# Kernel tuning notes

Hardware: AMD Instinct MI355X
Metric: run time of the kernel (lower is better)

Reference implementation:

```python
import jax, jax.numpy as jnp
import numpy as np

N_NODES = 20000
N_EDGES = 160000
N_GRAPHS = 500
F_IN = 128
HID = 512
N_CLS = 10
N_LAYERS = 3
BN_EPS = 1e-5
BN_BIAS = 1e-4  # BatchNorm1d weight init to 1, bias to 0.0001


def bn(x):
    # training-mode BatchNorm1d with gamma=1, beta=1e-4 (per module init)
    m = jnp.mean(x, axis=0)
    v = jnp.mean((x - m) ** 2, axis=0)
    return (x - m) * jax.lax.rsqrt(v + BN_EPS) + BN_BIAS


def gcn_norm(row, col, edge_weight, num_nodes):
    # add self loops with weight 1, symmetric deg^-1/2 normalization
    loop = jnp.arange(num_nodes)
    r = jnp.concatenate([row, loop])
    c = jnp.concatenate([col, loop])
    w = jnp.concatenate([edge_weight, jnp.ones((num_nodes,), edge_weight.dtype)])
    deg = jax.ops.segment_sum(w, r, num_segments=num_nodes)
    dis = jnp.where(deg > 0, jax.lax.rsqrt(deg), jnp.zeros_like(deg))
    return r, c, dis[r] * w * dis[c]


def gcn(x, W, b, r, c, norm):
    # x@W then gather source feats, scale by norm, scatter-add to targets
    h = x @ W
    out = jax.ops.segment_sum(norm[:, None] * h[c], r, num_segments=x.shape[0])
    return out + b


def readout(x, W1, b1, W2, b2):
    x = bn(x) @ W1 + b1
    x = jax.nn.relu(x)
    x = bn(x) @ W2 + b2
    return jax.nn.log_softmax(x, axis=-1)


def setup_inputs() -> dict:
    key = jax.random.key(0)
    ks = iter(jax.random.split(key, 40))

    def lin(k, fin, fout):
        return jax.random.normal(k, (fin, fout), jnp.float32) * (1.0 / np.sqrt(fin))

    x = jax.random.normal(next(ks), (N_NODES, F_IN), jnp.float32)
    edge_index = jax.random.randint(next(ks), (2, N_EDGES), 0, N_NODES)
    batch = jnp.sort(jax.random.randint(next(ks), (N_NODES,), 0, N_GRAPHS))
    perm = jax.random.permutation(next(ks), N_GRAPHS)

    inp = {"x": x, "edge_index": edge_index, "batch": batch, "perm": perm}
    inp["conv_feat_W"] = lin(next(ks), F_IN, HID)
    inp["conv_feat_b"] = jnp.zeros((HID,), jnp.float32)
    inp["convs_W"] = jax.random.normal(next(ks), (N_LAYERS, HID, HID), jnp.float32) * (1.0 / np.sqrt(HID))
    inp["convs_b"] = jnp.zeros((N_LAYERS, HID), jnp.float32)
    inp["edge_att_W"] = lin(next(ks), 2 * HID, 2)
    inp["edge_att_b"] = jnp.zeros((2,), jnp.float32)
    inp["node_att_W"] = lin(next(ks), HID, 2)
    inp["node_att_b"] = jnp.zeros((2,), jnp.float32)
    inp["ctx_W"] = lin(next(ks), HID, HID)
    inp["ctx_b"] = jnp.zeros((HID,), jnp.float32)
    inp["obj_W"] = lin(next(ks), HID, HID)
    inp["obj_b"] = jnp.zeros((HID,), jnp.float32)
    for tag in ("c", "o", "co"):
        inp[f"fc1_{tag}_W"] = lin(next(ks), HID, HID)
        inp[f"fc1_{tag}_b"] = jnp.zeros((HID,), jnp.float32)
        inp[f"fc2_{tag}_W"] = lin(next(ks), HID, N_CLS)
        inp[f"fc2_{tag}_b"] = jnp.zeros((N_CLS,), jnp.float32)
    return inp


def reference(x, edge_index, batch, perm,
              conv_feat_W, conv_feat_b, convs_W, convs_b,
              edge_att_W, edge_att_b, node_att_W, node_att_b,
              ctx_W, ctx_b, obj_W, obj_b,
              fc1_c_W, fc1_c_b, fc2_c_W, fc2_c_b,
              fc1_o_W, fc1_o_b, fc2_o_W, fc2_o_b,
              fc1_co_W, fc1_co_b, fc2_co_W, fc2_co_b):
    row, col = edge_index[0], edge_index[1]
    n = x.shape[0]

    x = bn(x)
    x = jax.nn.relu(x @ conv_feat_W + conv_feat_b)  # conv_feat has gfn=True: pure linear

    # unweighted symmetric norm, shared by all stacked convs
    r1, c1, nrm1 = gcn_norm(row, col, jnp.ones((row.shape[0],), x.dtype), n)
    for i in range(N_LAYERS):
        x = bn(x)
        x = jax.nn.relu(gcn(x, convs_W[i], convs_b[i], r1, c1, nrm1))

    edge_rep = jnp.concatenate([x[row], x[col]], axis=-1)        # [E, 2H]
    edge_att = jax.nn.softmax(edge_rep @ edge_att_W + edge_att_b, axis=-1)
    node_att = jax.nn.softmax(x @ node_att_W + node_att_b, axis=-1)

    xc = node_att[:, :1] * x
    xo = node_att[:, 1:] * x

    rc, cc, nc = gcn_norm(row, col, edge_att[:, 0], n)
    ro, co_, no_ = gcn_norm(row, col, edge_att[:, 1], n)
    xc = jax.nn.relu(gcn(bn(xc), ctx_W, ctx_b, rc, cc, nc))
    xo = jax.nn.relu(gcn(bn(xo), obj_W, obj_b, ro, co_, no_))

    xc = jax.ops.segment_sum(xc, batch, num_segments=N_GRAPHS)   # global_add_pool
    xo = jax.ops.segment_sum(xo, batch, num_segments=N_GRAPHS)

    xc_logis = readout(xc, fc1_c_W, fc1_c_b, fc2_c_W, fc2_c_b)
    xo_logis = readout(xo, fc1_o_W, fc1_o_b, fc2_o_W, fc2_o_b)
    # cat_or_add == 'add', with_random shuffle realized by perm
    xco_logis = readout(xc[perm] + xo, fc1_co_W, fc1_co_b, fc2_co_W, fc2_co_b)
    return xc_logis, xo_logis, xco_logis
```

## Files before the change

kernel.cpp:

```cpp
#include <hip/hip_runtime.h>
#include <stdint.h>

#define NN 20000
#define NE 160000
#define NG 500
#define FIN 128
#define HID 512
#define NCLS 10
#define BNG 256
#define NB3 32

typedef __attribute__((ext_vector_type(8))) short short8;
typedef __attribute__((ext_vector_type(4))) float f32x4;
typedef __attribute__((ext_vector_type(4))) unsigned short ushort4v;

__device__ __forceinline__ float bf2f(unsigned int u){
  union{unsigned int i; float f;} x; x.i = u<<16; return x.f;
}
__device__ __forceinline__ unsigned short f2bf(float f){
  union{float f; unsigned int i;} x; x.f=f;
  unsigned int r = x.i + 0x7fffu + ((x.i>>16)&1u);
  return (unsigned short)(r>>16);
}
__device__ __forceinline__ unsigned int pk2(float a, float b){
  return (unsigned int)f2bf(a) | ((unsigned int)f2bf(b) << 16);
}

__device__ __forceinline__ void gload16(unsigned short* lds, const unsigned short* g){
  __builtin_amdgcn_global_load_lds((const __attribute__((address_space(1))) unsigned int*)g,
                                   (__attribute__((address_space(3))) unsigned int*)lds,
                                   16, 0, 0);
}

__device__ __forceinline__ void fma8(float* acc, uint4 v, float w){
  acc[0] += w*bf2f(v.x & 0xffffu); acc[1] += w*bf2f(v.x >> 16);
  acc[2] += w*bf2f(v.y & 0xffffu); acc[3] += w*bf2f(v.y >> 16);
  acc[4] += w*bf2f(v.z & 0xffffu); acc[5] += w*bf2f(v.z >> 16);
  acc[6] += w*bf2f(v.w & 0xffffu); acc[7] += w*bf2f(v.w >> 16);
}

__global__ void sentinel_k(float* out){ out[0] = 12345.0f; }

struct W2BT { const float* src[9]; unsigned short* dst[9]; };
__global__ void setup_all(W2BT p, int* __restrict__ cnt, int* __restrict__ fillc,
                          float* __restrict__ degc, float* __restrict__ dego,
                          float* __restrict__ Sc, float* __restrict__ So,
                          float* __restrict__ stats6){
  int idx = blockIdx.x*blockDim.x + threadIdx.x;
  if (idx < FIN*HID + 8*HID*HID){
    int seg, off, K;
    if (idx < FIN*HID){ seg = 0; off = idx; K = FIN; }
    else {
      int r = idx - FIN*HID;
      seg = 1 + (r >> 18); off = r & (HID*HID-1); K = HID;
    }
    int k = off >> 9, n = off & 511;
    p.dst[seg][(size_t)n*K + k] = f2bf(p.src[seg][off]);
  }
  if (idx < NN){ cnt[idx]=0; fillc[idx]=0; degc[idx]=1.0f; dego[idx]=1.0f; Sc[idx]=0.f; So[idx]=0.f; }
  if (idx < 6*1024) stats6[idx] = 0.f;
}

__global__ __launch_bounds__(1024) void bnstats_p(const float* __restrict__ X, int M, int F,
                                                  float* __restrict__ partials){
  __shared__ float lds[1024*9];
  const int t = threadIdx.x;
  const int cg = F >> 2;
  const int cid = t & (cg-1);
  const int rid = t / cg;
  const int rpb = 1024 / cg;
  float s0=0,s1=0,s2=0,s3=0,q0=0,q1=0,q2=0,q3=0;
  const int rowsPer = (M + BNG - 1)/BNG;
  int r0 = blockIdx.x*rowsPer, r1 = r0 + rowsPer; if (r1 > M) r1 = M;
  for (int r = r0 + rid; r < r1; r += rpb){
    float4 v = *(const float4*)&X[(size_t)r*F + cid*4];
    s0+=v.x; q0+=v.x*v.x; s1+=v.y; q1+=v.y*v.y; s2+=v.z; q2+=v.z*v.z; s3+=v.w; q3+=v.w*v.w;
  }
  int base = (rid*cg + cid)*9;
  lds[base+0]=s0; lds[base+1]=s1; lds[base+2]=s2; lds[base+3]=s3;
  lds[base+4]=q0; lds[base+5]=q1; lds[base+6]=q2; lds[base+7]=q3;
  __syncthreads();
  if (t < cg*8){
    int ci = t >> 3, i = t & 7;
    float acc = 0.f;
    for (int g=0; g<rpb; ++g) acc += lds[(g*cg + ci)*9 + i];
    int col = ci*4 + (i & 3);
    partials[(size_t)blockIdx.x*(2*F) + ((i < 4) ? col : F + col)] = acc;
  }
}

__global__ __launch_bounds__(1024) void bnstats_dual(const unsigned short* __restrict__ X,
                                                     const float* __restrict__ na,
                                                     float* __restrict__ partials){
  __shared__ float lds[1024*17];
  const int t = threadIdx.x;
  const int cid = t & 127;
  const int rid = t >> 7;
  float sC[4]={0,0,0,0}, qC[4]={0,0,0,0}, sO[4]={0,0,0,0}, qO[4]={0,0,0,0};
  const int rowsPer = (NN + BNG - 1)/BNG;
  int r0 = blockIdx.x*rowsPer, r1 = r0 + rowsPer; if (r1 > NN) r1 = NN;
  for (int r = r0 + rid; r < r1; r += 8){
    float a0 = na[2*r], a1 = na[2*r+1];
    uint2 u = *(const uint2*)&X[(size_t)r*HID + cid*4];
    float e[4] = {bf2f(u.x & 0xffffu), bf2f(u.x >> 16), bf2f(u.y & 0xffffu), bf2f(u.y >> 16)};
#pragma unroll
    for (int i=0;i<4;i++){
      float vc = e[i]*a0, vo = e[i]*a1;
      sC[i]+=vc; qC[i]+=vc*vc; sO[i]+=vo; qO[i]+=vo*vo;
    }
  }
  int base = (rid*128 + cid)*17;
#pragma unroll
  for (int i=0;i<4;i++){
    lds[base+i]=sC[i]; lds[base+4+i]=qC[i]; lds[base+8+i]=sO[i]; lds[base+12+i]=qO[i];
  }
  __syncthreads();
  for (int idx = t; idx < 2048; idx += 1024){
    int ci = idx >> 4, i = idx & 15;
    float acc = 0.f;
    for (int g=0; g<8; ++g) acc += lds[(g*128 + ci)*17 + i];
    int grp = i >> 2, col = ci*4 + (i & 3);
    partials[(size_t)blockIdx.x*2048 + grp*HID + col] = acc;
  }
}

__global__ void bnfin_red(const float* __restrict__ partials, int stride, int off,
                          int M, int F, float* __restrict__ mstat){
  __shared__ float lds[4][64][2];
  int t = threadIdx.x;
  int cl = t & 63, ch = t >> 6;
  int c = blockIdx.x*64 + cl;
  float s = 0.f, q = 0.f;
  if (c < F){
    for (int b = ch*64; b < ch*64 + 64; ++b){
      s += partials[(size_t)b*stride + off + c];
      q += partials[(size_t)b*stride + off + F + c];
    }
  }
  lds[ch][cl][0] = s; lds[ch][cl][1] = q;
  __syncthreads();
  if (ch == 0 && c < F){
    s = lds[0][cl][0]+lds[1][cl][0]+lds[2][cl][0]+lds[3][cl][0];
    q = lds[0][cl][1]+lds[1][cl][1]+lds[2][cl][1]+lds[3][cl][1];
    float m = s/(float)M;
    float v = q/(float)M - m*m;
    mstat[c] = m;
    mstat[F+c] = rsqrtf(v + 1e-5f);
  }
}

__global__ void bnfin_red2(const float* __restrict__ partials, float* __restrict__ mstatCO){
  __shared__ float lds[4][64][2];
  int t = threadIdx.x;
  int cl = t & 63, ch = t >> 6;
  int c = blockIdx.x*64 + cl;
  int off = blockIdx.y*1024;
  float s = 0.f, q = 0.f;
  for (int b = ch*64; b < ch*64 + 64; ++b){
    s += partials[(size_t)b*2048 + off + c];
    q += partials[(size_t)b*2048 + off + HID + c];
  }
  lds[ch][cl][0] = s; lds[ch][cl][1] = q;
  __syncthreads();
  if (ch == 0){
    s = lds[0][cl][0]+lds[1][cl][0]+lds[2][cl][0]+lds[3][cl][0];
    q = lds[0][cl][1]+lds[1][cl][1]+lds[2][cl][1]+lds[3][cl][1];
    float m = s/(float)NN;
    float v = q/(float)NN - m*m;
    mstatCO[blockIdx.y*1024 + c] = m;
    mstatCO[blockIdx.y*1024 + HID + c] = rsqrtf(v + 1e-5f);
  }
}

__global__ void bncast(const float* __restrict__ X, const float* __restrict__ mstat,
                       int M, int F, unsigned short* __restrict__ out){
  int idx = blockIdx.x*blockDim.x + threadIdx.x;
  int total4 = M*F/4;
  if (idx >= total4) return;
  int base = idx*4;
  int c = base & (F-1);
  float4 v = *(const float4*)&X[base];
  ushort4v o;
  o[0] = f2bf((v.x - mstat[c+0])*mstat[F+c+0] + 1e-4f);
  o[1] = f2bf((v.y - mstat[c+1])*mstat[F+c+1] + 1e-4f);
  o[2] = f2bf((v.z - mstat[c+2])*mstat[F+c+2] + 1e-4f);
  o[3] = f2bf((v.w - mstat[c+3])*mstat[F+c+3] + 1e-4f);
  *(ushort4v*)&out[base] = o;
}

__global__ void csr_count(const int* __restrict__ ei, int* __restrict__ cnt){
  int e = blockIdx.x*blockDim.x + threadIdx.x;
  if (e < NE) atomicAdd(&cnt[ei[e]], 1);
}

__global__ __launch_bounds__(1024) void scan1(const int* __restrict__ cnt, int* __restrict__ rowp,
                                              float* __restrict__ dis1, int* __restrict__ bsum){
  __shared__ int buf[1024];
  int t = threadIdx.x;
  int i = blockIdx.x*1024 + t;
  int v = 0;
  if (i < NN){ v = cnt[i] + 1; dis1[i] = rsqrtf((float)v); }
  buf[t] = v;
  __syncthreads();
  for (int off=1; off<1024; off<<=1){
    int xv = (t >= off) ? buf[t-off] : 0;
    __syncthreads();
    buf[t] += xv;
    __syncthreads();
  }
  if (i < NN) rowp[i+1] = buf[t];
  if (t == 1023) bsum[blockIdx.x] = buf[1023];
}

__global__ __launch_bounds__(1024) void scan3(int* __restrict__ rowp, const int* __restrict__ bsum){
  __shared__ int base;
  int bx = blockIdx.x;
  if (threadIdx.x == 0){
    int a = 0;
    for (int b=0; b<bx; ++b) a += bsum[b];
    base = a;
  }
  __syncthreads();
  int i = bx*1024 + threadIdx.x;
  if (i < NN) rowp[i+1] += base;
  if (i == 0) rowp[0] = 0;
}

__global__ void csr_fill(const int* __restrict__ ei, const int* __restrict__ rowp,
                         const int* __restrict__ cnt, int* __restrict__ fillc,
                         const float* __restrict__ dis1,
                         int* __restrict__ ccol, int* __restrict__ crow, int* __restrict__ ceid,
                         int2* __restrict__ cw1){
  int id = blockIdx.x*blockDim.x + threadIdx.x;
  if (id < NE){
    int r = ei[id], c = ei[NE + id];
    int pos = atomicAdd(&fillc[r], 1);
    int idx = rowp[r] + pos;
    ccol[idx] = c; crow[idx] = r; ceid[idx] = id;
    cw1[idx] = make_int2(c, __float_as_int(dis1[r]*dis1[c]));
  } else if (id < NE + NN){
    int i = id - NE;
    int idx = rowp[i] + cnt[i];
    ccol[idx] = i; crow[idx] = i; ceid[idx] = -1;
    cw1[idx] = make_int2(i, __float_as_int(dis1[i]*dis1[i]));
  }
}

__global__ void att_node(const unsigned short* __restrict__ X, const float* __restrict__ nW,
                         const float* __restrict__ nb, const float* __restrict__ eW,
                         float* __restrict__ na, float* __restrict__ eab){
  __shared__ float wnl[1024], wet[1024], web[1024];
  int t = threadIdx.x;
  for (int i=t; i<1024; i+=256){ wnl[i]=nW[i]; wet[i]=eW[i]; web[i]=eW[1024+i]; }
  __syncthreads();
  int wv = blockIdx.x*4 + (t >> 6);
  int l = t & 63;
  uint4 u = ((const uint4*)(X + (size_t)wv*HID))[l];
  float xv[8] = {bf2f(u.x&0xffffu), bf2f(u.x>>16), bf2f(u.y&0xffffu), bf2f(u.y>>16),
                 bf2f(u.z&0xffffu), bf2f(u.z>>16), bf2f(u.w&0xffffu), bf2f(u.w>>16)};
  float s0=0,s1=0,s2=0,s3=0,s4=0,s5=0;
#pragma unroll
  for (int j=0; j<8; ++j){
    int k = l*8 + j;
    float x = xv[j];
    s0 += x * wnl[2*k];   s1 += x * wnl[2*k+1];
    s2 += x * wet[2*k];   s3 += x * wet[2*k+1];
    s4 += x * web[2*k];   s5 += x * web[2*k+1];
  }
  for (int m=1; m<64; m<<=1){
    s0 += __shfl_xor(s0,m); s1 += __shfl_xor(s1,m); s2 += __shfl_xor(s2,m);
    s3 += __shfl_xor(s3,m); s4 += __shfl_xor(s4,m); s5 += __shfl_xor(s5,m);
  }
  if (l == 0){
    float z0 = s0 + nb[0], z1 = s1 + nb[1];
    float mx = fmaxf(z0,z1);
    float e0 = expf(z0-mx), e1 = expf(z1-mx);
    float inv = 1.0f/(e0+e1);
    na[2*wv] = e0*inv; na[2*wv+1] = e1*inv;
    eab[4*wv] = s2; eab[4*wv+1] = s3; eab[4*wv+2] = s4; eab[4*wv+3] = s5;
  }
}

__global__ void att_edge(const int* __restrict__ ei, const float* __restrict__ eab,
                         const float* __restrict__ eb, float* __restrict__ att,
                         float* __restrict__ degc, float* __restrict__ dego){
  int e = blockIdx.x*blockDim.x + threadIdx.x;
  if (e >= NE) return;
  int r = ei[e], c = ei[NE+e];
  float z0 = eab[4*r]   + eab[4*c+2] + eb[0];
  float z1 = eab[4*r+1] + eab[4*c+3] + eb[1];
  float mx = fmaxf(z0,z1);
  float e0 = expf(z0-mx), e1 = expf(z1-mx);
  float inv = 1.0f/(e0+e1);
  float a0 = e0*inv, a1 = e1*inv;
  att[2*e] = a0; att[2*e+1] = a1;
  atomicAdd(&degc[r], a0);
  atomicAdd(&dego[r], a1);
}

__global__ void wco_kernel(const int* __restrict__ crow, const int* __restrict__ ccol,
                           const int* __restrict__ ceid, const float* __restrict__ att,
                           const float* __restrict__ degc, const float* __restrict__ dego,
                           const float* __restrict__ na,
                           float* __restrict__ wcv, float* __restrict__ wov,
                           float* __restrict__ Sc, float* __restrict__ So){
  int j = blockIdx.x*blockDim.x + threadIdx.x;
  if (j >= NE + NN) return;
  int r = crow[j], c = ccol[j], e = ceid[j];
  float a0 = (e < 0) ? 1.0f : att[2*e];
  float a1 = (e < 0) ? 1.0f : att[2*e+1];
  float wc = rsqrtf(degc[r]) * a0 * rsqrtf(degc[c]);
  float wo = rsqrtf(dego[r]) * a1 * rsqrtf(dego[c]);
  wcv[j] = wc * na[2*c];
  wov[j] = wo * na[2*c+1];
  atomicAdd(&Sc[r], wc);
  atomicAdd(&So[r], wo);
}

__global__ __launch_bounds__(256) void aggregate_bn(const unsigned short* __restrict__ A,
                                                    const int* __restrict__ rowp,
                                                    const int2* __restrict__ cw,
                                                    const float* __restrict__ stats,
                                                    float invM,
                                                    unsigned short* __restrict__ out){
  int row = blockIdx.x*4 + (threadIdx.x >> 6);
  int l = threadIdx.x & 63;
  const uint4* Av = (const uint4*)A;
  int s = rowp[row], e = rowp[row+1];
  float acc[8] = {0,0,0,0,0,0,0,0};
  float sw = 0.f;
  int j = s;
  for (; j+3 < e; j += 4){
    int2 p0 = cw[j], p1 = cw[j+1], p2 = cw[j+2], p3 = cw[j+3];
    float w0 = __int_as_float(p0.y), w1 = __int_as_float(p1.y);
    float w2 = __int_as_float(p2.y), w3 = __int_as_float(p3.y);
    uint4 v0 = Av[(size_t)p0.x*64 + l];
    uint4 v1 = Av[(size_t)p1.x*64 + l];
    uint4 v2 = Av[(size_t)p2.x*64 + l];
    uint4 v3 = Av[(size_t)p3.x*64 + l];
    fma8(acc, v0, w0); fma8(acc, v1, w1); fma8(acc, v2, w2); fma8(acc, v3, w3);
    sw += w0 + w1 + w2 + w3;
  }
  for (; j < e; ++j){
    int2 p = cw[j];
    float w = __int_as_float(p.y);
    uint4 v = Av[(size_t)p.x*64 + l];
    fma8(acc, v, w);
    sw += w;
  }
  float g[8];
#pragma unroll
  for (int i=0;i<8;i++){
    int c = l*8 + i;
    float m = stats[c]*invM;
    float rs = rsqrtf(stats[512+c]*invM - m*m + 1e-5f);
    g[i] = rs*acc[i] + sw*(1e-4f - m*rs);
  }
  uint4 o;
  o.x = pk2(g[0],g[1]); o.y = pk2(g[2],g[3]); o.z = pk2(g[4],g[5]); o.w = pk2(g[6],g[7]);
  ((uint4*)out)[(size_t)row*64 + l] = o;
}

__global__ __launch_bounds__(256) void aggregate_dual(const unsigned short* __restrict__ A,
                                                      const int* __restrict__ rowp,
                                                      const int* __restrict__ ccol,
                                                      const float* __restrict__ wc,
                                                      const float* __restrict__ wo,
                                                      const float* __restrict__ Sc,
                                                      const float* __restrict__ So,
                                                      const float* __restrict__ mstatCO,
                                                      unsigned short* __restrict__ outC,
                                                      unsigned short* __restrict__ outO){
  int row = blockIdx.x*4 + (threadIdx.x >> 6);
  int l = threadIdx.x & 63;
  const uint4* Av = (const uint4*)A;
  int s = rowp[row], e = rowp[row+1];
  float aC[8] = {0,0,0,0,0,0,0,0};
  float aO[8] = {0,0,0,0,0,0,0,0};
  int j = s;
  for (; j+3 < e; j += 4){
    int c0 = ccol[j], c1 = ccol[j+1], c2 = ccol[j+2], c3 = ccol[j+3];
    float wc0=wc[j], wc1=wc[j+1], wc2=wc[j+2], wc3=wc[j+3];
    float wo0=wo[j], wo1=wo[j+1], wo2=wo[j+2], wo3=wo[j+3];
    uint4 v0 = Av[(size_t)c0*64 + l];
    uint4 v1 = Av[(size_t)c1*64 + l];
    uint4 v2 = Av[(size_t)c2*64 + l];
    uint4 v3 = Av[(size_t)c3*64 + l];
    fma8(aC, v0, wc0); fma8(aO, v0, wo0);
    fma8(aC, v1, wc1); fma8(aO, v1, wo1);
    fma8(aC, v2, wc2); fma8(aO, v2, wo2);
    fma8(aC, v3, wc3); fma8(aO, v3, wo3);
  }
  for (; j < e; ++j){
    uint4 v = Av[(size_t)ccol[j]*64 + l];
    fma8(aC, v, wc[j]); fma8(aO, v, wo[j]);
  }
  float ScR = Sc[row], SoR = So[row];
  float gC[8], gO[8];
#pragma unroll
  for (int i=0;i<8;i++){
    int c = l*8 + i;
    float mc = mstatCO[c],      rc = mstatCO[512+c];
    float mo = mstatCO[1024+c], ro = mstatCO[1536+c];
    gC[i] = rc*aC[i] + ScR*(1e-4f - mc*rc);
    gO[i] = ro*aO[i] + SoR*(1e-4f - mo*ro);
  }
  uint4 oc, oo;
  oc.x = pk2(gC[0],gC[1]); oc.y = pk2(gC[2],gC[3]); oc.z = pk2(gC[4],gC[5]); oc.w = pk2(gC[6],gC[7]);
  oo.x = pk2(gO[0],gO[1]); oo.y = pk2(gO[2],gO[3]); oo.z = pk2(gO[4],gO[5]); oo.w = pk2(gO[6],gO[7]);
  ((uint4*)outC)[(size_t)row*64 + l] = oc;
  ((uint4*)outO)[(size_t)row*64 + l] = oo;
}

__global__ __launch_bounds__(256) void gemm_bt(const unsigned short* __restrict__ A,
                                               const unsigned short* __restrict__ Bt,
                                               unsigned short* __restrict__ O,
                                               const float* __restrict__ bias,
                                               float* __restrict__ stats,
                                               int M, int K, int relu, int split,
                                               const unsigned short* A2,
                                               const unsigned short* Bt2,
                                               unsigned short* O2,
                                               const float* bias2){
  __shared__ unsigned short As[2][128*32];
  __shared__ unsigned short Bs[2][128*32];
  const int tid = threadIdx.x;
  const int w = tid >> 6, l = tid & 63;
  int bx = blockIdx.x;
  if (split && bx >= split){ A = A2; Bt = Bt2; O = O2; bias = bias2; bx -= split; }
  const int m0 = bx*128, n0 = blockIdx.y*128;
  const int wm = w >> 1, wn = w & 1;
  const int lr = l & 15, lh = l >> 4;

  f32x4 acc[4][4];
#pragma unroll
  for (int i=0;i<4;i++)
#pragma unroll
    for (int j=0;j<4;j++) acc[i][j] = 0.0f;

  const int q0 = w*2, q1 = w*2+1;
  const int sub = l >> 2;
  const int kc  = (l & 3)*8;
  int ma0 = m0 + q0*16 + sub; if (ma0 >= M) ma0 = M-1;
  int ma1 = m0 + q1*16 + sub; if (ma1 >= M) ma1 = M-1;
  const int nb0 = n0 + q0*16 + sub;
  const int nb1 = n0 + q1*16 + sub;
  const unsigned short* Ar0 = A + (size_t)ma0*K + kc;
  const unsigned short* Ar1 = A + (size_t)ma1*K + kc;
  const unsigned short* Br0 = Bt + (size_t)nb0*K + kc;
  const unsigned short* Br1 = Bt + (size_t)nb1*K + kc;

  const int NT = K >> 5;
  gload16(&As[0][q0*512], Ar0);
  gload16(&As[0][q1*512], Ar1);
  gload16(&Bs[0][q0*512], Br0);
  gload16(&Bs[0][q1*512], Br1);
  int cur = 0;
  for (int t=0; t<NT; ++t){
    if (t+1 < NT){
      int k1 = (t+1) << 5;
      gload16(&As[cur^1][q0*512], Ar0 + k1);
      gload16(&As[cur^1][q1*512], Ar1 + k1);
      gload16(&Bs[cur^1][q0*512], Br0 + k1);
      gload16(&Bs[cur^1][q1*512], Br1 + k1);
      asm volatile("s_waitcnt vmcnt(4)" ::: "memory");
    } else {
      asm volatile("s_waitcnt vmcnt(0)" ::: "memory");
    }
    __builtin_amdgcn_s_barrier();
    asm volatile("" ::: "memory");
    short8 af[4], bfr[4];
#pragma unroll
    for (int fm=0; fm<4; ++fm) af[fm]  = *(const short8*)&As[cur][(wm*64 + fm*16 + lr)*32 + lh*8];
#pragma unroll
    for (int fn=0; fn<4; ++fn) bfr[fn] = *(const short8*)&Bs[cur][(wn*64 + fn*16 + lr)*32 + lh*8];
#pragma unroll
    for (int fm=0; fm<4; ++fm)
#pragma unroll
      for (int fn=0; fn<4; ++fn)
        acc[fm][fn] = __builtin_amdgcn_mfma_f32_16x16x32_bf16(af[fm], bfr[fn], acc[fm][fn], 0, 0, 0);
    asm volatile("" ::: "memory");
    __builtin_amdgcn_s_barrier();
    asm volatile("" ::: "memory");
    cur ^= 1;
  }
  float bv[4], cs[4]={0,0,0,0}, cq[4]={0,0,0,0};
  int col[4];
#pragma unroll
  for (int fn=0; fn<4; ++fn){ col[fn] = n0 + wn*64 + fn*16 + lr; bv[fn] = bias[col[fn]]; }
#pragma unroll
  for (int fm=0; fm<4; ++fm){
#pragma unroll
    for (int j=0; j<4; ++j){
      int row = m0 + wm*64 + fm*16 + lh*4 + j;
      if (row < M){
#pragma unroll
        for (int fn=0; fn<4; ++fn){
          float v = acc[fm][fn][j] + bv[fn];
          if (relu) v = fmaxf(v, 0.f);
          O[(size_t)row*HID + col[fn]] = f2bf(v);
          cs[fn] += v; cq[fn] += v*v;
        }
      }
    }
  }
  if (stats){
#pragma unroll
    for (int m=16; m<64; m<<=1){
#pragma unroll
      for (int fn=0; fn<4; ++fn){ cs[fn] += __shfl_xor(cs[fn], m); cq[fn] += __shfl_xor(cq[fn], m); }
    }
    if (lh == 0){
#pragma unroll
      for (int fn=0; fn<4; ++fn){
        atomicAdd(&stats[col[fn]], cs[fn]);
        atomicAdd(&stats[512+col[fn]], cq[fn]);
      }
    }
  }
}

struct FC1P { const unsigned short* Bt[3]; const float* bias[3]; };
__global__ __launch_bounds__(256) void gemm_fc1(const unsigned short* __restrict__ A, FC1P p,
                                                unsigned short* __restrict__ O,
                                                float* __restrict__ statsB){
  __shared__ unsigned short As[2][128*32];
  __shared__ unsigned short Bs[2][128*32];
  const int tid = threadIdx.x;
  const int w = tid >> 6, l = tid & 63;
  const int m0 = blockIdx.x*128, n0 = blockIdx.y*128;
  const int branch = blockIdx.x >> 2;
  const unsigned short* Bt = p.Bt[branch];
  const float* bias = p.bias[branch];
  float* stats = statsB + branch*1024;
  const int K = HID;
  const int wm = w >> 1, wn = w & 1;
  const int lr = l & 15, lh = l >> 4;

  f32x4 acc[4][4];
#pragma unroll
  for (int i=0;i<4;i++)
#pragma unroll
    for (int j=0;j<4;j++) acc[i][j] = 0.0f;

  const int q0 = w*2, q1 = w*2+1;
  const int sub = l >> 2;
  const int kc  = (l & 3)*8;
  const int ma0 = m0 + q0*16 + sub;
  const int ma1 = m0 + q1*16 + sub;
  const int nb0 = n0 + q0*16 + sub;
  const int nb1 = n0 + q1*16 + sub;
  const unsigned short* Ar0 = A + (size_t)ma0*K + kc;
  const unsigned short* Ar1 = A + (size_t)ma1*K + kc;
  const unsigned short* Br0 = Bt + (size_t)nb0*K + kc;
  const unsigned short* Br1 = Bt + (size_t)nb1*K + kc;

  const int NT = K >> 5;
  gload16(&As[0][q0*512], Ar0);
  gload16(&As[0][q1*512], Ar1);
  gload16(&Bs[0][q0*512], Br0);
  gload16(&Bs[0][q1*512], Br1);
  int cur = 0;
  for (int t=0; t<NT; ++t){
    if (t+1 < NT){
      int k1 = (t+1) << 5;
      gload16(&As[cur^1][q0*512], Ar0 + k1);
      gload16(&As[cur^1][q1*512], Ar1 + k1);
      gload16(&Bs[cur^1][q0*512], Br0 + k1);
      gload16(&Bs[cur^1][q1*512], Br1 + k1);
      asm volatile("s_waitcnt vmcnt(4)" ::: "memory");
    } else {
      asm volatile("s_waitcnt vmcnt(0)" ::: "memory");
    }
    __builtin_amdgcn_s_barrier();
    asm volatile("" ::: "memory");
    short8 af[4], bfr[4];
#pragma unroll
    for (int fm=0; fm<4; ++fm) af[fm]  = *(const short8*)&As[cur][(wm*64 + fm*16 + lr)*32 + lh*8];
#pragma unroll
    for (int fn=0; fn<4; ++fn) bfr[fn] = *(const short8*)&Bs[cur][(wn*64 + fn*16 + lr)*32 + lh*8];
#pragma unroll
    for (int fm=0; fm<4; ++fm)
#pragma unroll
      for (int fn=0; fn<4; ++fn)
        acc[fm][fn] = __builtin_amdgcn_mfma_f32_16x16x32_bf16(af[fm], bfr[fn], acc[fm][fn], 0, 0, 0);
    asm volatile("" ::: "memory");
    __builtin_amdgcn_s_barrier();
    asm volatile("" ::: "memory");
    cur ^= 1;
  }
  float bv[4], cs[4]={0,0,0,0}, cq[4]={0,0,0,0};
  int col[4];
#pragma unroll
  for (int fn=0; fn<4; ++fn){ col[fn] = n0 + wn*64 + fn*16 + lr; bv[fn] = bias[col[fn]]; }
#pragma unroll
  for (int fm=0; fm<4; ++fm){
#pragma unroll
    for (int j=0; j<4; ++j){
      int row = m0 + wm*64 + fm*16 + lh*4 + j;
      bool real = (row & 511) < NG;
#pragma unroll
      for (int fn=0; fn<4; ++fn){
        float v = fmaxf(acc[fm][fn][j] + bv[fn], 0.f);
        O[(size_t)row*HID + col[fn]] = f2bf(v);
        if (real){ cs[fn] += v; cq[fn] += v*v; }
      }
    }
  }
#pragma unroll
  for (int m=16; m<64; m<<=1){
#pragma unroll
    for (int fn=0; fn<4; ++fn){ cs[fn] += __shfl_xor(cs[fn], m); cq[fn] += __shfl_xor(cq[fn], m); }
  }
  if (lh == 0){
#pragma unroll
    for (int fn=0; fn<4; ++fn){
      atomicAdd(&stats[col[fn]], cs[fn]);
      atomicAdd(&stats[512+col[fn]], cq[fn]);
    }
  }
}

__global__ void pool2(const unsigned short* __restrict__ XC, const unsigned short* __restrict__ XO,
                      const int* __restrict__ batch, float* __restrict__ gc, float* __restrict__ go){
  int g = blockIdx.x;
  int t = threadIdx.x;
  const unsigned short* X = blockIdx.y ? XO : XC;
  float* out = blockIdx.y ? go : gc;
  int lo = 0, hi = NN;
  while (lo < hi){ int mid = (lo+hi) >> 1; if (batch[mid] < g) lo = mid+1; else hi = mid; }
  int s = lo;
  lo = 0; hi = NN;
  while (lo < hi){ int mid = (lo+hi) >> 1; if (batch[mid] < g+1) lo = mid+1; else hi = mid; }
  int e = lo;
  float a0 = 0.f, a1 = 0.f;
  for (int i=s; i<e; ++i){
    unsigned int v = *(const unsigned int*)&X[(size_t)i*HID + t*2];
    a0 += bf2f(v & 0xffffu); a1 += bf2f(v >> 16);
  }
  out[(size_t)g*HID + t*2]     = a0;
  out[(size_t)g*HID + t*2 + 1] = a1;
}

__global__ __launch_bounds__(256) void bnstats3(const float* __restrict__ gc, const float* __restrict__ go,
                                                const int* __restrict__ perm, float* __restrict__ partials){
  __shared__ float lds[256*9];
  int br = blockIdx.y;
  int t = threadIdx.x;
  int cid = t & 127, rid = t >> 7;
  float s[4]={0,0,0,0}, q[4]={0,0,0,0};
  const int rowsPer = (NG + NB3 - 1)/NB3;
  int r0 = blockIdx.x*rowsPer, r1 = r0 + rowsPer; if (r1 > NG) r1 = NG;
  for (int r = r0 + rid; r < r1; r += 2){
    float4 v;
    if (br == 0)      v = *(const float4*)&gc[(size_t)r*HID + cid*4];
    else if (br == 1) v = *(const float4*)&go[(size_t)r*HID + cid*4];
    else {
      int ps = perm[r];
      float4 a = *(const float4*)&gc[(size_t)ps*HID + cid*4];
      float4 b = *(const float4*)&go[(size_t)r*HID + cid*4];
      v = make_float4(a.x+b.x, a.y+b.y, a.z+b.z, a.w+b.w);
    }
    float e[4] = {v.x, v.y, v.z, v.w};
#pragma unroll
    for (int i=0;i<4;i++){ s[i]+=e[i]; q[i]+=e[i]*e[i]; }
  }
  int base = (rid*128 + cid)*9;
#pragma unroll
  for (int i=0;i<4;i++){ lds[base+i]=s[i]; lds[base+4+i]=q[i]; }
  __syncthreads();
  for (int o = t; o < 1024; o += 256){
    int issq = o >> 9, col = o & 511;
    int ci = col >> 2, i = col & 3;
    float acc = lds[(0*128 + ci)*9 + issq*4 + i] + lds[(1*128 + ci)*9 + issq*4 + i];
    partials[(size_t)(br*NB3 + blockIdx.x)*1024 + issq*512 + col] = acc;
  }
}

__global__ void bnfin3(const float* __restrict__ partials, float* __restrict__ mstat3){
  __shared__ float lds[4][64][2];
  int t = threadIdx.x;
  int cl = t & 63, ch = t >> 6;
  int c = blockIdx.x*64 + cl;
  int br = blockIdx.y;
  float s = 0.f, q = 0.f;
  for (int b = ch*8; b < ch*8 + 8; ++b){
    s += partials[(size_t)(br*NB3 + b)*1024 + c];
    q += partials[(size_t)(br*NB3 + b)*1024 + 512 + c];
  }
  lds[ch][cl][0] = s; lds[ch][cl][1] = q;
  __syncthreads();
  if (ch == 0){
    s = lds[0][cl][0]+lds[1][cl][0]+lds[2][cl][0]+lds[3][cl][0];
    q = lds[0][cl][1]+lds[1][cl][1]+lds[2][cl][1]+lds[3][cl][1];
    float m = s/(float)NG;
    float v = q/(float)NG - m*m;
    mstat3[br*1024 + c] = m;
    mstat3[br*1024 + 512 + c] = rsqrtf(v + 1e-5f);
  }
}

__global__ void bncast3(const float* __restrict__ gc, const float* __restrict__ go,
                        const int* __restrict__ perm, const float* __restrict__ mstat3,
                        unsigned short* __restrict__ out){
  int idx = blockIdx.x*blockDim.x + threadIdx.x;
  if (idx >= 1536*128) return;
  int r = idx >> 7;
  int cg = idx & 127;
  int br = r >> 9, lr = r & 511;
  ushort4v o;
  if (lr >= NG){ o[0]=0; o[1]=0; o[2]=0; o[3]=0; }
  else {
    float4 v;
    if (br == 0)      v = *(const float4*)&gc[(size_t)lr*HID + cg*4];
    else if (br == 1) v = *(const float4*)&go[(size_t)lr*HID + cg*4];
    else {
      int ps = perm[lr];
      float4 a = *(const float4*)&gc[(size_t)ps*HID + cg*4];
      float4 b = *(const float4*)&go[(size_t)lr*HID + cg*4];
      v = make_float4(a.x+b.x, a.y+b.y, a.z+b.z, a.w+b.w);
    }
    const float* ms = mstat3 + br*1024;
    int c = cg*4;
    o[0] = f2bf((v.x - ms[c+0])*ms[512+c+0] + 1e-4f);
    o[1] = f2bf((v.y - ms[c+1])*ms[512+c+1] + 1e-4f);
    o[2] = f2bf((v.z - ms[c+2])*ms[512+c+2] + 1e-4f);
    o[3] = f2bf((v.w - ms[c+3])*ms[512+c+3] + 1e-4f);
  }
  *(ushort4v*)&out[(size_t)r*HID + cg*4] = o;
}

struct ROP { const float* W2[3]; const float* b2[3]; };
__global__ void readout_final3(const unsigned short* __restrict__ T, const float* __restrict__ statsB,
                               float invM, ROP p, float* __restrict__ out){
  int g = blockIdx.x;
  int br = blockIdx.y;
  int l = threadIdx.x;
  const float* stats = statsB + br*1024;
  const float* W2 = p.W2[br];
  const float* b2 = p.b2[br];
  float acc[NCLS];
#pragma unroll
  for (int c=0; c<NCLS; ++c) acc[c] = 0.f;
  uint4 u = ((const uint4*)(T + (size_t)(br*512 + g)*HID))[l];
  float xv[8] = {bf2f(u.x&0xffffu), bf2f(u.x>>16), bf2f(u.y&0xffffu), bf2f(u.y>>16),
                 bf2f(u.z&0xffffu), bf2f(u.z>>16), bf2f(u.w&0xffffu), bf2f(u.w>>16)};
#pragma unroll
  for (int j=0; j<8; ++j){
    int k = l*8 + j;
    float m = stats[k]*invM;
    float rs = rsqrtf(stats[512+k]*invM - m*m + 1e-5f);
    float v = (xv[j] - m)*rs + 1e-4f;
#pragma unroll
    for (int c=0; c<NCLS; ++c) acc[c] += v * W2[k*NCLS + c];
  }
  for (int m=1; m<64; m<<=1){
#pragma unroll
    for (int c=0; c<NCLS; ++c) acc[c] += __shfl_xor(acc[c], m);
  }
  if (l == 0){
    float z[NCLS];
    float mx = -1e30f;
#pragma unroll
    for (int c=0; c<NCLS; ++c){ z[c] = acc[c] + b2[c]; mx = fmaxf(mx, z[c]); }
    float s = 0.f;
#pragma unroll
    for (int c=0; c<NCLS; ++c) s += expf(z[c]-mx);
    float lse = mx + logf(s);
#pragma unroll
    for (int c=0; c<NCLS; ++c) out[(size_t)(br*NG + g)*NCLS + c] = z[c] - lse;
  }
}

extern "C" void kernel_launch(void* const* d_in, const int* in_sizes, int n_in,
                              void* d_out, int out_size, void* d_ws, size_t ws_size,
                              hipStream_t stream){
  (void)in_sizes; (void)n_in; (void)out_size;
  const float* x      = (const float*)d_in[0];
  const int*   ei     = (const int*)d_in[1];
  const int*   batch  = (const int*)d_in[2];
  const int*   perm   = (const int*)d_in[3];
  const float* convfW = (const float*)d_in[4];
  const float* convfB = (const float*)d_in[5];
  const float* convsW = (const float*)d_in[6];
  const float* convsB = (const float*)d_in[7];
  const float* eattW  = (const float*)d_in[8];
  const float* eattB  = (const float*)d_in[9];
  const float* nattW  = (const float*)d_in[10];
  const float* nattB  = (const float*)d_in[11];
  const float* ctxW   = (const float*)d_in[12];
  const float* ctxB   = (const float*)d_in[13];
  const float* objW   = (const float*)d_in[14];
  const float* objB   = (const float*)d_in[15];
  const float* fc1W[3] = {(const float*)d_in[16], (const float*)d_in[20], (const float*)d_in[24]};
  const float* fc1B[3] = {(const float*)d_in[17], (const float*)d_in[21], (const float*)d_in[25]};
  const float* fc2W[3] = {(const float*)d_in[18], (const float*)d_in[22], (const float*)d_in[26]};
  const float* fc2B[3] = {(const float*)d_in[19], (const float*)d_in[23], (const float*)d_in[27]};
  float* out = (float*)d_out;

  char* p = (char*)d_ws;
  auto alloc = [&](size_t bytes)->char*{ char* r = p; p += (bytes + 255) & ~((size_t)255); return r; };
  const int T = NE + NN;
  unsigned short* Xbf = (unsigned short*)alloc((size_t)NN*HID*2);
  unsigned short* Gbf = (unsigned short*)alloc((size_t)NN*HID*2);
  unsigned short* GbfO= (unsigned short*)alloc((size_t)NN*HID*2);
  unsigned short* XbfO= (unsigned short*)alloc((size_t)NN*HID*2);
  unsigned short* Abf = (unsigned short*)alloc((size_t)NN*FIN*2);
  unsigned short* WtF = (unsigned short*)alloc((size_t)HID*FIN*2);
  unsigned short* WtL = (unsigned short*)alloc((size_t)3*HID*HID*2);
  unsigned short* WtC = (unsigned short*)alloc((size_t)HID*HID*2);
  unsigned short* WtO = (unsigned short*)alloc((size_t)HID*HID*2);
  unsigned short* WtR = (unsigned short*)alloc((size_t)3*HID*HID*2);
  int* cnt   = (int*)alloc((size_t)NN*4);
  int* fillc = (int*)alloc((size_t)NN*4);
  int* rowp  = (int*)alloc((size_t)(NN+1)*4);
  int* bsum  = (int*)alloc(32*4);
  int* ccol  = (int*)alloc((size_t)T*4);
  int* crow  = (int*)alloc((size_t)T*4);
  int* ceid  = (int*)alloc((size_t)T*4);
  int2* cw1  = (int2*)alloc((size_t)T*8);
  float* wcv = (float*)alloc((size_t)T*4);
  float* wov = (float*)alloc((size_t)T*4);
  float* dis1 = (float*)alloc((size_t)NN*4);
  float* degc = (float*)alloc((size_t)NN*4);
  float* dego = (float*)alloc((size_t)NN*4);
  float* Sc   = (float*)alloc((size_t)NN*4);
  float* So   = (float*)alloc((size_t)NN*4);
  float* stats6 = (float*)alloc(6*1024*4);
  float* mstat  = (float*)alloc(2*HID*4);
  float* mstatCO= (float*)alloc(2*1024*4);
  float* mstat3 = (float*)alloc(3*1024*4);
  float* na   = (float*)alloc((size_t)NN*2*4);
  float* eab  = (float*)alloc((size_t)NN*4*4);
  float* att  = (float*)alloc((size_t)NE*2*4);
  float* gc   = (float*)alloc((size_t)NG*HID*4);
  float* go   = (float*)alloc((size_t)NG*HID*4);
  float* part = (float*)alloc((size_t)BNG*2048*4);
  if ((size_t)(p - (char*)d_ws) > ws_size){
    sentinel_k<<<1,1,0,stream>>>(out);
    return;
  }
  unsigned short* Abf3 = Abf;
  unsigned short* Gbf3 = GbfO;
  const float invNN = 1.0f/(float)NN;
  const float invNG = 1.0f/(float)NG;

  W2BT wp;
  wp.src[0]=convfW; wp.dst[0]=WtF;
  for (int i=0;i<3;i++){ wp.src[1+i]=convsW+(size_t)i*HID*HID; wp.dst[1+i]=WtL+(size_t)i*HID*HID; }
  wp.src[4]=ctxW; wp.dst[4]=WtC;
  wp.src[5]=objW; wp.dst[5]=WtO;
  for (int i=0;i<3;i++){ wp.src[6+i]=fc1W[i]; wp.dst[6+i]=WtR+(size_t)i*HID*HID; }
  setup_all<<<(FIN*HID + 8*HID*HID + 255)/256, 256, 0, stream>>>(wp, cnt, fillc, degc, dego, Sc, So, stats6);

  csr_count<<<(NE+255)/256,256,0,stream>>>(ei, cnt);
  scan1<<<(NN+1023)/1024,1024,0,stream>>>(cnt, rowp, dis1, bsum);
  scan3<<<(NN+1023)/1024,1024,0,stream>>>(rowp, bsum);
  csr_fill<<<(T+255)/256,256,0,stream>>>(ei, rowp, cnt, fillc, dis1, ccol, crow, ceid, cw1);

  bnstats_p<<<BNG,1024,0,stream>>>(x, NN, FIN, part);
  bnfin_red<<<(FIN+63)/64,256,0,stream>>>(part, 2*FIN, 0, NN, FIN, mstat);
  bncast<<<((NN*FIN/4)+255)/256,256,0,stream>>>(x, mstat, NN, FIN, Abf);
  gemm_bt<<<dim3((NN+127)/128,4),256,0,stream>>>(Abf, WtF, Xbf, convfB, stats6, NN, FIN, 1,
                                                 0, nullptr, nullptr, nullptr, nullptr);

  for (int i=0;i<3;i++){
    aggregate_bn<<<NN/4,256,0,stream>>>(Xbf, rowp, cw1, stats6 + i*1024, invNN, Gbf);
    gemm_bt<<<dim3((NN+127)/128,4),256,0,stream>>>(Gbf, WtL+(size_t)i*HID*HID, Xbf,
                                                   convsB+(size_t)i*HID,
                                                   (i<2) ? (stats6 + (i+1)*1024) : nullptr,
                                                   NN, HID, 1, 0, nullptr, nullptr, nullptr, nullptr);
  }

  att_node<<<NN/4,256,0,stream>>>(Xbf, nattW, nattB, eattW, na, eab);
  att_edge<<<(NE+255)/256,256,0,stream>>>(ei, eab, eattB, att, degc, dego);
  wco_kernel<<<(T+255)/256,256,0,stream>>>(crow, ccol, ceid, att, degc, dego, na, wcv, wov, Sc, So);

  bnstats_dual<<<BNG,1024,0,stream>>>(Xbf, na, part);
  bnfin_red2<<<dim3(8,2),256,0,stream>>>(part, mstatCO);
  aggregate_dual<<<NN/4,256,0,stream>>>(Xbf, rowp, ccol, wcv, wov, Sc, So, mstatCO, Gbf, GbfO);
  {
    const int gx = (NN+127)/128;
    gemm_bt<<<dim3(2*gx,4),256,0,stream>>>(Gbf, WtC, Xbf, ctxB, nullptr, NN, HID, 1,
                                           gx, GbfO, WtO, XbfO, objB);
  }
  pool2<<<dim3(NG,2),256,0,stream>>>(Xbf, XbfO, batch, gc, go);

  bnstats3<<<dim3(NB3,3),256,0,stream>>>(gc, go, perm, part);
  bnfin3<<<dim3(8,3),256,0,stream>>>(part, mstat3);
  bncast3<<<(1536*128+255)/256,256,0,stream>>>(gc, go, perm, mstat3, Abf3);
  FC1P fp;
  for (int i=0;i<3;i++){ fp.Bt[i] = WtR+(size_t)i*HID*HID; fp.bias[i] = fc1B[i]; }
  gemm_fc1<<<dim3(12,4),256,0,stream>>>(Abf3, fp, Gbf3, stats6 + 3*1024);
  ROP rp;
  for (int i=0;i<3;i++){ rp.W2[i] = fc2W[i]; rp.b2[i] = fc2B[i]; }
  readout_final3<<<dim3(NG,3),64,0,stream>>>(Gbf3, stats6 + 3*1024, invNG, rp, out);
}
```

Baseline: 476.6 us.

## Stage GEMM epilogue through LDS for coalesced stores and XCD-aware block swizzle

The GEMM epilogue now writes bf16 results into a padded shared-memory tile and then stores full rows with 16-byte vector writes, replacing scattered 2-byte global stores. The launch becomes a 1D grid whose block index is remapped so that consecutive tiles land on the same XCD and share A rows in L2. Shared memory moves to dynamic allocation sized for the output tile (about 34 KB), and the double-buffered A/B tiles reuse that space. The extra sync and larger LDS footprint may lower occupancy.

```diff
diff --git a/kernel.cpp b/kernel.cpp
--- a/kernel.cpp
+++ b/kernel.cpp
@@ -422,13 +422,21 @@
                                                const unsigned short* Bt2,
                                                unsigned short* O2,
                                                const float* bias2){
-  __shared__ unsigned short As[2][128*32];
-  __shared__ unsigned short Bs[2][128*32];
+  extern __shared__ unsigned short smem[];
+  unsigned short* As0 = smem;
+  unsigned short* Bs0 = smem + 8192;
+  unsigned short* Cs  = smem;
   const int tid = threadIdx.x;
   const int w = tid >> 6, l = tid & 63;
-  int bx = blockIdx.x;
-  if (split && bx >= split){ A = A2; Bt = Bt2; O = O2; bias = bias2; bx -= split; }
-  const int m0 = bx*128, n0 = blockIdx.y*128;
+
+  int lin = blockIdx.x;
+  int total = gridDim.x;
+  int q = total >> 3, r = total & 7;
+  int xcd = lin & 7, idx = lin >> 3;
+  int swz = (xcd < r ? xcd*(q+1) : r*(q+1) + (xcd - r)*q) + idx;
+  if (split && swz >= split){ A = A2; Bt = Bt2; O = O2; bias = bias2; swz -= split; }
+  const int m0 = (swz >> 2)*128, n0 = (swz & 3)*128;
+
   const int wm = w >> 1, wn = w & 1;
   const int lr = l & 15, lh = l >> 4;
 
@@ -451,18 +459,18 @@
   const unsigned short* Br1 = Bt + (size_t)nb1*K + kc;
 
   const int NT = K >> 5;
-  gload16(&As[0][q0*512], Ar0);
-  gload16(&As[0][q1*512], Ar1);
-  gload16(&Bs[0][q0*512], Br0);
-  gload16(&Bs[0][q1*512], Br1);
+  gload16(&As0[q0*512], Ar0);
+  gload16(&As0[q1*512], Ar1);
+  gload16(&Bs0[q0*512], Br0);
+  gload16(&Bs0[q1*512], Br1);
   int cur = 0;
   for (int t=0; t<NT; ++t){
     if (t+1 < NT){
       int k1 = (t+1) << 5;
-      gload16(&As[cur^1][q0*512], Ar0 + k1);
-      gload16(&As[cur^1][q1*512], Ar1 + k1);
-      gload16(&Bs[cur^1][q0*512], Br0 + k1);
-      gload16(&Bs[cur^1][q1*512], Br1 + k1);
+      gload16(&As0[(cur^1)*4096 + q0*512], Ar0 + k1);
+      gload16(&As0[(cur^1)*4096 + q1*512], Ar1 + k1);
+      gload16(&Bs0[(cur^1)*4096 + q0*512], Br0 + k1);
+      gload16(&Bs0[(cur^1)*4096 + q1*512], Br1 + k1);
       asm volatile("s_waitcnt vmcnt(4)" ::: "memory");
     } else {
       asm volatile("s_waitcnt vmcnt(0)" ::: "memory");
@@ -471,9 +479,9 @@
     asm volatile("" ::: "memory");
     short8 af[4], bfr[4];
 #pragma unroll
-    for (int fm=0; fm<4; ++fm) af[fm]  = *(const short8*)&As[cur][(wm*64 + fm*16 + lr)*32 + lh*8];
-#pragma unroll
-    for (int fn=0; fn<4; ++fn) bfr[fn] = *(const short8*)&Bs[cur][(wn*64 + fn*16 + lr)*32 + lh*8];
+    for (int fm=0; fm<4; ++fm) af[fm]  = *(const short8*)&As0[cur*4096 + (wm*64 + fm*16 + lr)*32 + lh*8];
+#pragma unroll
+    for (int fn=0; fn<4; ++fn) bfr[fn] = *(const short8*)&Bs0[cur*4096 + (wn*64 + fn*16 + lr)*32 + lh*8];
 #pragma unroll
     for (int fm=0; fm<4; ++fm)
 #pragma unroll
@@ -492,17 +500,25 @@
   for (int fm=0; fm<4; ++fm){
 #pragma unroll
     for (int j=0; j<4; ++j){
-      int row = m0 + wm*64 + fm*16 + lh*4 + j;
-      if (row < M){
-#pragma unroll
-        for (int fn=0; fn<4; ++fn){
-          float v = acc[fm][fn][j] + bv[fn];
-          if (relu) v = fmaxf(v, 0.f);
-          O[(size_t)row*HID + col[fn]] = f2bf(v);
-          cs[fn] += v; cq[fn] += v*v;
-        }
+      int trow = wm*64 + fm*16 + lh*4 + j;
+      bool valid = (m0 + trow) < M;
+#pragma unroll
+      for (int fn=0; fn<4; ++fn){
+        float v = acc[fm][fn][j] + bv[fn];
+        if (relu) v = fmaxf(v, 0.f);
+        Cs[trow*136 + wn*64 + fn*16 + lr] = f2bf(v);
+        if (valid){ cs[fn] += v; cq[fn] += v*v; }
       }
     }
+  }
+  __syncthreads();
+#pragma unroll
+  for (int i=0;i<8;i++){
+    int trow = i*16 + (tid>>4);
+    int colb = (tid&15)*8;
+    uint4 vv = *(const uint4*)&Cs[trow*136 + colb];
+    int grow = m0 + trow;
+    if (grow < M) *(uint4*)&O[(size_t)grow*HID + n0 + colb] = vv;
   }
   if (stats){
 #pragma unroll
@@ -844,6 +860,7 @@
   unsigned short* Gbf3 = GbfO;
   const float invNN = 1.0f/(float)NN;
   const float invNG = 1.0f/(float)NG;
+  const int GEMM_LDS = 128*136*2;
 
   W2BT wp;
   wp.src[0]=convfW; wp.dst[0]=WtF;
@@ -858,18 +875,20 @@
   scan3<<<(NN+1023)/1024,1024,0,stream>>>(rowp, bsum);
   csr_fill<<<(T+255)/256,256,0,stream>>>(ei, rowp, cnt, fillc, dis1, ccol, crow, ceid, cw1);
 
+  const int NBLK = ((NN+127)/128)*4;
+
   bnstats_p<<<BNG,1024,0,stream>>>(x, NN, FIN, part);
   bnfin_red<<<(FIN+63)/64,256,0,stream>>>(part, 2*FIN, 0, NN, FIN, mstat);
   bncast<<<((NN*FIN/4)+255)/256,256,0,stream>>>(x, mstat, NN, FIN, Abf);
-  gemm_bt<<<dim3((NN+127)/128,4),256,0,stream>>>(Abf, WtF, Xbf, convfB, stats6, NN, FIN, 1,
-                                                 0, nullptr, nullptr, nullptr, nullptr);
+  gemm_bt<<<NBLK,256,GEMM_LDS,stream>>>(Abf, WtF, Xbf, convfB, stats6, NN, FIN, 1,
+                                        0, nullptr, nullptr, nullptr, nullptr);
 
   for (int i=0;i<3;i++){
     aggregate_bn<<<NN/4,256,0,stream>>>(Xbf, rowp, cw1, stats6 + i*1024, invNN, Gbf);
-    gemm_bt<<<dim3((NN+127)/128,4),256,0,stream>>>(Gbf, WtL+(size_t)i*HID*HID, Xbf,
-                                                   convsB+(size_t)i*HID,
-                                                   (i<2) ? (stats6 + (i+1)*1024) : nullptr,
-                                                   NN, HID, 1, 0, nullptr, nullptr, nullptr, nullptr);
+    gemm_bt<<<NBLK,256,GEMM_LDS,stream>>>(Gbf, WtL+(size_t)i*HID*HID, Xbf,
+                                          convsB+(size_t)i*HID,
+                                          (i<2) ? (stats6 + (i+1)*1024) : nullptr,
+                                          NN, HID, 1, 0, nullptr, nullptr, nullptr, nullptr);
   }
 
   att_node<<<NN/4,256,0,stream>>>(Xbf, nattW, nattB, eattW, na, eab);
@@ -879,11 +898,8 @@
   bnstats_dual<<<BNG,1024,0,stream>>>(Xbf, na, part);
   bnfin_red2<<<dim3(8,2),256,0,stream>>>(part, mstatCO);
   aggregate_dual<<<NN/4,256,0,stream>>>(Xbf, rowp, ccol, wcv, wov, Sc, So, mstatCO, Gbf, GbfO);
-  {
-    const int gx = (NN+127)/128;
-    gemm_bt<<<dim3(2*gx,4),256,0,stream>>>(Gbf, WtC, Xbf, ctxB, nullptr, NN, HID, 1,
-                                           gx, GbfO, WtO, XbfO, objB);
-  }
+  gemm_bt<<<2*NBLK,256,GEMM_LDS,stream>>>(Gbf, WtC, Xbf, ctxB, nullptr, NN, HID, 1,
+                                          NBLK, GbfO, WtO, XbfO, objB);
   pool2<<<dim3(NG,2),256,0,stream>>>(Xbf, XbfO, batch, gc, go);
 
   bnstats3<<<dim3(NB3,3),256,0,stream>>>(gc, go, perm, part);
```

Measured after the change: 442.6 us. -7.1%, faster.
